# Kernel optimization log

Measured on AMD Instinct MI355X. Metric: run time of the kernel, lower is better.

Reference implementation:

```python
import jax, jax.numpy as jnp
import numpy as np

D_MODEL, H, D_K, D_V, D_FF = 1024, 16, 64, 64, 4096
B, L = 2, 2048
EPS = 1e-5


def layer_norm(x, g, b):
    mu = jnp.mean(x, axis=-1, keepdims=True)
    var = jnp.mean(jnp.square(x - mu), axis=-1, keepdims=True)
    return (x - mu) * jax.lax.rsqrt(var + EPS) * g + b


def setup_inputs() -> dict:
    key = jax.random.key(0)
    ks = jax.random.split(key, 12)
    s = 0.02
    x = jax.random.normal(ks[0], (B, L, D_MODEL), dtype=jnp.float32)
    Wq = jax.random.normal(ks[1], (H, D_MODEL, D_K), dtype=jnp.float32) * s
    Wk = jax.random.normal(ks[2], (H, D_MODEL, D_K), dtype=jnp.float32) * s
    Wv = jax.random.normal(ks[3], (H, D_MODEL, D_V), dtype=jnp.float32) * s
    bq = jnp.zeros((H, D_K), dtype=jnp.float32)
    bk = jnp.zeros((H, D_K), dtype=jnp.float32)
    bv = jnp.zeros((H, D_V), dtype=jnp.float32)
    Wo = jax.random.normal(ks[4], (H * D_V, D_MODEL), dtype=jnp.float32) * s
    W1 = jax.random.normal(ks[5], (D_MODEL, D_FF), dtype=jnp.float32) * s
    b1 = jnp.zeros((D_FF,), dtype=jnp.float32)
    W2 = jax.random.normal(ks[6], (D_FF, D_MODEL), dtype=jnp.float32) * s
    ln1_g = jnp.ones((D_MODEL,), dtype=jnp.float32)
    ln1_b = jnp.zeros((D_MODEL,), dtype=jnp.float32)
    ln2_g = jnp.ones((D_MODEL,), dtype=jnp.float32)
    ln2_b = jnp.zeros((D_MODEL,), dtype=jnp.float32)
    return dict(x=x, Wq=Wq, bq=bq, Wk=Wk, bk=bk, Wv=Wv, bv=bv, Wo=Wo,
                ln1_g=ln1_g, ln1_b=ln1_b, W1=W1, b1=b1, W2=W2,
                ln2_g=ln2_g, ln2_b=ln2_b)


def reference(x, Wq, bq, Wk, bk, Wv, bv, Wo, ln1_g, ln1_b, W1, b1, W2, ln2_g, ln2_b):
    # Batched multi-head attention (all heads at once, equivalent to the
    # per-head Python loop in the original module).
    Q = jnp.einsum('bld,hdk->bhlk', x, Wq) + bq[None, :, None, :]
    K = jnp.einsum('bld,hdk->bhlk', x, Wk) + bk[None, :, None, :]
    V = jnp.einsum('bld,hdv->bhlv', x, Wv) + bv[None, :, None, :]
    scores = jnp.einsum('bhlk,bhmk->bhlm', Q, K) * (1.0 / jnp.sqrt(jnp.float32(D_K)))
    attn = jax.nn.softmax(scores, axis=-1)
    O = jnp.einsum('bhlm,bhmv->bhlv', attn, V)        # [b,h,l,dv]
    O = jnp.transpose(O, (0, 2, 1, 3)).reshape(x.shape[0], x.shape[1], H * D_V)
    mha = O @ Wo                                       # [b,l,d_model]
    # residual + LayerNorm (dropout_prob=0 -> identity)
    h1 = layer_norm(x + mha, ln1_g, ln1_b)
    ff = jax.nn.relu(h1 @ W1 + b1) @ W2
    return layer_norm(h1 + ff, ln2_g, ln2_b)
```

## Files before the change

### kernel.cpp

```cpp
#include <hip/hip_runtime.h>

typedef unsigned short u16;
typedef unsigned int u32;
typedef short bf16x8 __attribute__((ext_vector_type(8)));
typedef float f32x4 __attribute__((ext_vector_type(4)));
typedef unsigned int u32x2 __attribute__((ext_vector_type(2)));
typedef unsigned int u32x4 __attribute__((ext_vector_type(4)));

#define D_MODEL 1024
#define NH 16
#define DK 64
#define DFF 4096
#define BATCH 2
#define SEQ 2048
#define BL (BATCH*SEQ)
#define NQKV 3072
#define Q_SCALE 0.18033688011f

__device__ __forceinline__ float bfraw2f(u16 u) {
    union { u32 i; float f; } c; c.i = ((u32)u) << 16; return c.f;
}
__device__ __forceinline__ u16 f2bfraw(float f) {
    union { float f; u32 i; } c; c.f = f;
    u32 i = c.i;
    u32 lsb = (i >> 16) & 1u;
    i += 0x7fffu + lsb;
    return (u16)(i >> 16);
}
__device__ __forceinline__ u32 fasu(float f) {
    union { float f; u32 i; } c; c.f = f; return c.i;
}
__device__ __forceinline__ u32 pack_bf2(float lo, float hi) {
    return __builtin_amdgcn_perm(fasu(hi) + 0x8000u, fasu(lo) + 0x8000u,
                                 0x07060302u);
}
__device__ __forceinline__ void gload_lds16(const u16* g, u16* l) {
    __builtin_amdgcn_global_load_lds(
        (const __attribute__((address_space(1))) void*)g,
        (__attribute__((address_space(3))) void*)l, 16, 0, 0);
}

__global__ __launch_bounds__(256) void cast_f32_bf16(const float* __restrict__ in,
                                                     u16* __restrict__ out) {
    int i = (blockIdx.x * 256 + threadIdx.x) * 4;
    f32x4 v = *(const f32x4*)&in[i];
#pragma unroll
    for (int j = 0; j < 4; j++) out[i + j] = f2bfraw(v[j]);
}


__global__ __launch_bounds__(256) void transpose2d(const float* __restrict__ in,
                                                   u16* __restrict__ out,
                                                   int R, int C) {
    __shared__ u16 t[64][65];
    int c0 = blockIdx.x * 64, r0 = blockIdx.y * 64;
    int col = threadIdx.x & 63, rr = threadIdx.x >> 6;
    for (int i = rr; i < 64; i += 4)
        t[i][col] = f2bfraw(in[(size_t)(r0 + i) * C + c0 + col]);
    __syncthreads();
    for (int i = rr; i < 64; i += 4)
        out[(size_t)(c0 + i) * R + r0 + col] = t[col][i];
}

__global__ __launch_bounds__(256) void transpose_wqkv(const float* __restrict__ Wq,
                                                      const float* __restrict__ Wk,
                                                      const float* __restrict__ Wv,
                                                      u16* __restrict__ out) {
    __shared__ u16 t[64][65];
    int d0 = blockIdx.x * 64;
    int h = blockIdx.y;
    int ms = blockIdx.z;
    const float* W = (ms == 0) ? Wq : (ms == 1) ? Wk : Wv;
    const float* src = W + (size_t)h * D_MODEL * DK;
    int col = threadIdx.x & 63, rr = threadIdx.x >> 6;
    for (int i = rr; i < 64; i += 4)
        t[i][col] = f2bfraw(src[(size_t)(d0 + i) * DK + col]);
    __syncthreads();
    u16* dst = out + (size_t)(ms * 1024 + h * 64) * D_MODEL;
    for (int i = rr; i < 64; i += 4)
        dst[(size_t)i * D_MODEL + d0 + col] = t[col][i];
}

__global__ __launch_bounds__(256) void concat_bias(const float* __restrict__ bq,
                                                   const float* __restrict__ bk,
                                                   const float* __restrict__ bv,
                                                   float* __restrict__ out) {
    int i = blockIdx.x * 256 + threadIdx.x;
    out[i] = (i < 1024) ? bq[i] : (i < 2048) ? bk[i - 1024] : bv[i - 2048];
}


template <int BM, int BN, int T, int OUT_F32, int RELU, int HASBIAS, int SPLITK,
          int SCALEQ, int VSTORE>
__global__ __launch_bounds__(T, 2) void gemm3(const u16* __restrict__ A,
                                              const u16* __restrict__ Bt,
                                              const float* __restrict__ bias,
                                              void* __restrict__ Cout,
                                              u16* __restrict__ vtout,
                                              int M, int N, int K) {
    constexpr int WGN = BN / 64;
    constexpr int WGM = (T / 64) / WGN;
    constexpr int PWM = BM / WGM;
    constexpr int MF = PWM / 16;
    __shared__ __attribute__((aligned(16))) u16 As[2][BM * 64];
    __shared__ __attribute__((aligned(16))) u16 Bs[2][BN * 64];
    const int tid = threadIdx.x;
    const int lane = tid & 63, wid = tid >> 6;
    const int quad = lane >> 4, l16 = lane & 15;

    int nwg = gridDim.x * gridDim.y;
    int flat = blockIdx.y * gridDim.x + blockIdx.x;
    if ((nwg & 7) == 0) {
        int q = nwg >> 3;
        flat = (flat & 7) * q + (flat >> 3);
    }
    const int m0 = (flat % gridDim.x) * BM;
    const int n0 = (flat / gridDim.x) * BN;

    const int z = (SPLITK > 1) ? blockIdx.z : 0;
    const int Klen = K / SPLITK;
    const int NT = Klen / 64;
    const int kb0 = z * Klen;

    const int wrow = (wid / WGN) * PWM;
    const int wcol = (wid % WGN) * 64;

    f32x4 acc[MF][4];
#pragma unroll
    for (int i = 0; i < MF; i++)
#pragma unroll
        for (int j = 0; j < 4; j++) acc[i][j] = (f32x4){0.f, 0.f, 0.f, 0.f};

    auto stage = [&](int kb, int slot) {
#pragma unroll
        for (int p = 0; p < (BM * 8) / T; p++) {
            int ew = p * T + wid * 64;
            int e = ew + lane;
            int row = e >> 3, ch = e & 7;
            gload_lds16(&A[(size_t)(m0 + row) * K + kb + ((ch ^ (row & 7)) * 8)],
                        &As[slot][ew * 8]);
        }
#pragma unroll
        for (int p = 0; p < (BN * 8) / T; p++) {
            int ew = p * T + wid * 64;
            int e = ew + lane;
            int row = e >> 3, ch = e & 7;
            gload_lds16(&Bt[(size_t)(n0 + row) * K + kb + ((ch ^ (row & 7)) * 8)],
                        &Bs[slot][ew * 8]);
        }
    };

    stage(kb0, 0);
    if (NT > 1) stage(kb0 + 64, 1);

    for (int t = 0; t < NT; t++) {
        if (t + 1 < NT) {
            asm volatile("s_waitcnt vmcnt(8)" ::: "memory");
        } else {
            asm volatile("s_waitcnt vmcnt(0)" ::: "memory");
        }
        __builtin_amdgcn_s_barrier();
        __builtin_amdgcn_sched_barrier(0);

        const u16* as = As[t & 1];
        const u16* bs = Bs[t & 1];
        __builtin_amdgcn_s_setprio(1);
        bf16x8 bfr[4][2];
#pragma unroll
        for (int j = 0; j < 4; j++) {
            int rb = wcol + j * 16 + l16;
#pragma unroll
            for (int kh = 0; kh < 2; kh++)
                bfr[j][kh] = *(const bf16x8*)&bs[rb * 64 + (((kh * 4 + quad) ^ (rb & 7)) * 8)];
        }
#pragma unroll
        for (int i = 0; i < MF; i++) {
            int ra = wrow + i * 16 + l16;
            bf16x8 a0 = *(const bf16x8*)&as[ra * 64 + ((quad ^ (ra & 7)) * 8)];
            bf16x8 a1 = *(const bf16x8*)&as[ra * 64 + (((4 + quad) ^ (ra & 7)) * 8)];
#pragma unroll
            for (int j = 0; j < 4; j++) {
                acc[i][j] = __builtin_amdgcn_mfma_f32_16x16x32_bf16(a0, bfr[j][0], acc[i][j], 0, 0, 0);
                acc[i][j] = __builtin_amdgcn_mfma_f32_16x16x32_bf16(a1, bfr[j][1], acc[i][j], 0, 0, 0);
            }
        }
        __builtin_amdgcn_s_setprio(0);
        __builtin_amdgcn_sched_barrier(0);
        __builtin_amdgcn_s_barrier();
        __builtin_amdgcn_sched_barrier(0);
        if (t + 2 < NT) stage(kb0 + (t + 2) * 64, t & 1);
    }

    if (VSTORE && n0 >= 2048) {
#pragma unroll
        for (int i = 0; i < MF; i++) {
            int row0 = m0 + wrow + i * 16 + quad * 4;
            int bb = row0 >> 11, l = row0 & 2047;
#pragma unroll
            for (int j = 0; j < 4; j++) {
                int col = n0 + wcol + j * 16 + l16;
                float bv = HASBIAS ? bias[col] : 0.f;
                int dv = col - 2048;
                u32x2 w;
                w.x = pack_bf2(acc[i][j][0] + bv, acc[i][j][1] + bv);
                w.y = pack_bf2(acc[i][j][2] + bv, acc[i][j][3] + bv);
                *(u32x2*)&vtout[((size_t)(bb * 1024 + dv)) * 2048 + l] = w;
            }
        }
        return;
    }

    float* outf = (float*)Cout + (size_t)z * M * N;
#pragma unroll
    for (int i = 0; i < MF; i++) {
#pragma unroll
        for (int j = 0; j < 4; j++) {
#pragma unroll
            for (int r = 0; r < 4; r++) {
                int row = m0 + wrow + i * 16 + quad * 4 + r;
                int col = n0 + wcol + j * 16 + l16;
                float v = acc[i][j][r];
                if (HASBIAS) v += bias[col];
                if (RELU) v = v > 0.f ? v : 0.f;
                if (SCALEQ && col < 1024) v *= Q_SCALE;
                if (OUT_F32)
                    outf[(size_t)row * N + col] = v;
                else
                    ((u16*)Cout)[(size_t)row * N + col] = f2bfraw(v);
            }
        }
    }
}

__global__ __launch_bounds__(512, 4) void attn_kernel(const u16* __restrict__ qkv,
                                                      const u16* __restrict__ vt,
                                                      u16* __restrict__ O) {
    __shared__ __attribute__((aligned(16))) u16 Ks[2][128 * 64];
    __shared__ __attribute__((aligned(16))) u16 Vs[64 * 128];

    const int tid = threadIdx.x;
    const int lane = tid & 63, wid = tid >> 6;
    const int quad = lane >> 4, l16 = lane & 15;
    const int sw = l16 & 7;
    const int b = blockIdx.z, h = blockIdx.y;
    const int q0 = blockIdx.x * 128 + wid * 16;

    const size_t qrow = (size_t)(b * SEQ + q0 + l16) * NQKV + h * DK;
    const bf16x8 qf0 = *(const bf16x8*)&qkv[qrow + quad * 8];
    const bf16x8 qf1 = *(const bf16x8*)&qkv[qrow + 32 + quad * 8];

    const u16* Kbase = qkv + (size_t)(b * SEQ) * NQKV + D_MODEL + h * DK;
    const u16* Vbase = vt + (size_t)((b * NH + h) * DK) * SEQ;

    f32x4 oacc[4];
#pragma unroll
    for (int d = 0; d < 4; d++) oacc[d] = (f32x4){0.f, 0.f, 0.f, 0.f};
    float lr = 0.f;
    const f32x4 Z = {0.f, 0.f, 0.f, 0.f};

    auto stage_k = [&](int kt2, int buf) {
#pragma unroll
        for (int p = 0; p < 2; p++) {
            int seg = p * 8 + wid;
            int row = seg * 8 + (lane >> 3);
            int chunk = (lane & 7) ^ (lane >> 3);
            gload_lds16(&Kbase[(size_t)(kt2 + row) * NQKV + chunk * 8],
                        &Ks[buf][seg * 512]);
        }
    };
    bf16x8 vreg[2];
    auto load_v = [&](int kt2) {
#pragma unroll
        for (int p = 0; p < 2; p++) {
            int s = p * 512 + tid;
            vreg[p] = *(const bf16x8*)&Vbase[(size_t)(s >> 4) * SEQ + kt2 + (s & 15) * 8];
        }
    };
    stage_k(0, 0);
    load_v(0);

    for (int t = 0; t < SEQ / 128; t++) {
        const int kt = t * 128;
#pragma unroll
        for (int p = 0; p < 2; p++) {
            int s = p * 512 + tid;
            int vr = s >> 4, vc = s & 15;
            int chunkA = (vc >> 2) * 4 + (vc & 1) * 2;
            int rem = ((vc >> 1) & 1) * 4;
            u32x4 kv = __builtin_bit_cast(u32x4, vreg[p]);
            *(u32x2*)&Vs[vr * 128 + ((chunkA ^ (vr & 7)) * 8) + rem] =
                (u32x2){kv.x, kv.y};
            *(u32x2*)&Vs[vr * 128 + (((chunkA + 1) ^ (vr & 7)) * 8) + rem] =
                (u32x2){kv.z, kv.w};
        }
        __syncthreads();

        if (t + 1 < SEQ / 128) {
            stage_k(kt + 128, (t + 1) & 1);
            load_v(kt + 128);
        }

        const u16* kb = Ks[t & 1];

        f32x4 sacc[8];
        __builtin_amdgcn_s_setprio(1);
#pragma unroll
        for (int nt = 0; nt < 8; nt++) {
            const u16* krow = &kb[(nt * 16 + l16) * 64];
            bf16x8 kf0 = *(const bf16x8*)&krow[(quad ^ sw) * 8];
            bf16x8 kf1 = *(const bf16x8*)&krow[((4 + quad) ^ sw) * 8];
            f32x4 s0 = __builtin_amdgcn_mfma_f32_16x16x32_bf16(kf0, qf0, Z, 0, 0, 0);
            sacc[nt] = __builtin_amdgcn_mfma_f32_16x16x32_bf16(kf1, qf1, s0, 0, 0, 0);
        }
        __builtin_amdgcn_s_setprio(0);

        u32 wreg[8][2];
#pragma unroll
        for (int nt = 0; nt < 8; nt++) {
            float p0 = __builtin_amdgcn_exp2f(sacc[nt][0]);
            float p1 = __builtin_amdgcn_exp2f(sacc[nt][1]);
            float p2 = __builtin_amdgcn_exp2f(sacc[nt][2]);
            float p3 = __builtin_amdgcn_exp2f(sacc[nt][3]);
            lr += (p0 + p1) + (p2 + p3);
            wreg[nt][0] = pack_bf2(p0, p1);
            wreg[nt][1] = pack_bf2(p2, p3);
        }

        __builtin_amdgcn_s_setprio(1);
#pragma unroll
        for (int ks = 0; ks < 4; ks++) {
            u32x4 pw = (u32x4){wreg[2 * ks][0], wreg[2 * ks][1],
                               wreg[2 * ks + 1][0], wreg[2 * ks + 1][1]};
            bf16x8 pf = __builtin_bit_cast(bf16x8, pw);
#pragma unroll
            for (int d = 0; d < 4; d++) {
                bf16x8 vf = *(const bf16x8*)&Vs[(d * 16 + l16) * 128 +
                                                (((ks * 4 + quad) ^ sw) * 8)];
                oacc[d] = __builtin_amdgcn_mfma_f32_16x16x32_bf16(vf, pf, oacc[d], 0, 0, 0);
            }
        }
        __builtin_amdgcn_s_setprio(0);
        __syncthreads();
    }

    lr += __shfl_xor(lr, 16, 64);
    lr += __shfl_xor(lr, 32, 64);
    float iv = 1.f / lr;

    size_t row = (size_t)(b * SEQ + q0 + l16);
#pragma unroll
    for (int d = 0; d < 4; d++) {
        float o0 = oacc[d][0] * iv, o1 = oacc[d][1] * iv;
        float o2 = oacc[d][2] * iv, o3 = oacc[d][3] * iv;
        u32x2 w;
        w.x = ((u32)f2bfraw(o1) << 16) | f2bfraw(o0);
        w.y = ((u32)f2bfraw(o3) << 16) | f2bfraw(o2);
        *(u32x2*)&O[row * D_MODEL + h * DK + d * 16 + quad * 4] = w;
    }
}

__global__ __launch_bounds__(256) void ln3_kernel(const float* __restrict__ xa,
                                                  const float* __restrict__ xb,
                                                  const float* __restrict__ xc,
                                                  const float* __restrict__ g,
                                                  const float* __restrict__ be,
                                                  u16* __restrict__ out_bf,
                                                  float* __restrict__ out_f) {
    int row = blockIdx.x;
    int tid = threadIdx.x;
    const float* pa = xa + (size_t)row * D_MODEL;
    const float* pb = xb + (size_t)row * D_MODEL;
    const float* pc = xc + (size_t)row * D_MODEL;
    int c = tid * 4;
    f32x4 av = *(const f32x4*)&pa[c];
    f32x4 bv = *(const f32x4*)&pb[c];
    f32x4 cv = *(const f32x4*)&pc[c];
    float v[4];
    float s = 0.f, ss = 0.f;
#pragma unroll
    for (int i = 0; i < 4; i++) {
        v[i] = av[i] + bv[i] + cv[i];
        s += v[i];
        ss += v[i] * v[i];
    }
#pragma unroll
    for (int off = 32; off; off >>= 1) {
        s += __shfl_down(s, off, 64);
        ss += __shfl_down(ss, off, 64);
    }
    __shared__ float red[8];
    int wid = tid >> 6, lane = tid & 63;
    if (lane == 0) { red[wid] = s; red[4 + wid] = ss; }
    __syncthreads();
    if (tid == 0) {
        red[0] = red[0] + red[1] + red[2] + red[3];
        red[4] = red[4] + red[5] + red[6] + red[7];
    }
    __syncthreads();
    float mu = red[0] * (1.f / D_MODEL);
    float var = red[4] * (1.f / D_MODEL) - mu * mu;
    float rs = rsqrtf(var + 1e-5f);
#pragma unroll
    for (int i = 0; i < 4; i++) {
        float o = (v[i] - mu) * rs * g[c + i] + be[c + i];
        if (out_f) out_f[(size_t)row * D_MODEL + c + i] = o;
        if (out_bf) out_bf[(size_t)row * D_MODEL + c + i] = f2bfraw(o);
    }
}

extern "C" void kernel_launch(void* const* d_in, const int* in_sizes, int n_in,
                              void* d_out, int out_size, void* d_ws, size_t ws_size,
                              hipStream_t stream) {
    const float* x   = (const float*)d_in[0];
    const float* Wq  = (const float*)d_in[1];
    const float* bq  = (const float*)d_in[2];
    const float* Wk  = (const float*)d_in[3];
    const float* bk  = (const float*)d_in[4];
    const float* Wv  = (const float*)d_in[5];
    const float* bv  = (const float*)d_in[6];
    const float* Wo  = (const float*)d_in[7];
    const float* g1  = (const float*)d_in[8];
    const float* be1 = (const float*)d_in[9];
    const float* W1  = (const float*)d_in[10];
    const float* b1  = (const float*)d_in[11];
    const float* W2  = (const float*)d_in[12];
    const float* g2  = (const float*)d_in[13];
    const float* be2 = (const float*)d_in[14];

    char* w = (char*)d_ws;
    auto alloc = [&](size_t bytes) {
        char* p = w;
        w += (bytes + 255) & ~(size_t)255;
        return p;
    };
    u16* wqkv_t = (u16*)alloc((size_t)NQKV * D_MODEL * 2);
    u16* wo_t   = (u16*)alloc((size_t)D_MODEL * D_MODEL * 2);
    u16* w1_t   = (u16*)alloc((size_t)DFF * D_MODEL * 2);
    u16* w2_t   = (u16*)alloc((size_t)D_MODEL * DFF * 2);
    float* bqkv = (float*)alloc((size_t)NQKV * 4);
    u16* x_bf   = (u16*)alloc((size_t)BL * D_MODEL * 2);
    u16* qkvbuf = (u16*)alloc((size_t)BL * NQKV * 2);
    u16* vtbuf  = (u16*)alloc((size_t)BATCH * NH * DK * SEQ * 2);
    u16* obuf   = (u16*)alloc((size_t)BL * D_MODEL * 2);
    float* mha_p = (float*)alloc((size_t)2 * BL * D_MODEL * 4);
    u16* h1_bf  = (u16*)alloc((size_t)BL * D_MODEL * 2);
    float* h1_f = (float*)alloc((size_t)BL * D_MODEL * 4);
    u16* ffa    = (u16*)alloc((size_t)BL * DFF * 2);
    float* ffb_p = (float*)alloc((size_t)2 * BL * D_MODEL * 4);

    cast_f32_bf16<<<dim3(BL * D_MODEL / 1024), 256, 0, stream>>>(x, x_bf);
    transpose_wqkv<<<dim3(16, 16, 3), 256, 0, stream>>>(Wq, Wk, Wv, wqkv_t);
    transpose2d<<<dim3(16, 16), 256, 0, stream>>>(Wo, wo_t, 1024, 1024);
    transpose2d<<<dim3(64, 16), 256, 0, stream>>>(W1, w1_t, 1024, 4096);
    transpose2d<<<dim3(16, 64), 256, 0, stream>>>(W2, w2_t, 4096, 1024);
    concat_bias<<<dim3(12), 256, 0, stream>>>(bq, bk, bv, bqkv);

    gemm3<256, 256, 512, 0, 0, 1, 1, 1, 1><<<dim3(16, 12), 512, 0, stream>>>(
        x_bf, wqkv_t, bqkv, qkvbuf, vtbuf, BL, NQKV, D_MODEL);
    attn_kernel<<<dim3(16, 16, 2), 512, 0, stream>>>(qkvbuf, vtbuf, obuf);
    gemm3<128, 128, 256, 1, 0, 0, 2, 0, 0><<<dim3(32, 8, 2), 256, 0, stream>>>(
        obuf, wo_t, nullptr, mha_p, nullptr, BL, D_MODEL, D_MODEL);
    ln3_kernel<<<dim3(BL), 256, 0, stream>>>(x, mha_p, mha_p + (size_t)BL * D_MODEL,
                                             g1, be1, h1_bf, h1_f);
    gemm3<256, 256, 512, 0, 1, 1, 1, 0, 0><<<dim3(16, 16), 512, 0, stream>>>(
        h1_bf, w1_t, b1, ffa, nullptr, BL, DFF, D_MODEL);
    gemm3<128, 128, 256, 1, 0, 0, 2, 0, 0><<<dim3(32, 8, 2), 256, 0, stream>>>(
        ffa, w2_t, nullptr, ffb_p, nullptr, BL, D_MODEL, DFF);
    ln3_kernel<<<dim3(BL), 256, 0, stream>>>(h1_f, ffb_p, ffb_p + (size_t)BL * D_MODEL,
                                             g2, be2, nullptr, (float*)d_out);
}
```

Measured before the change: 369.7 us.

## Restructure GEMM main loop to 4-stage 32-wide K pipeline with split staging

```diff
diff --git a/kernel.cpp b/kernel.cpp
--- a/kernel.cpp
+++ b/kernel.cpp
@@ -92,7 +92,7 @@
 
 template <int BM, int BN, int T, int OUT_F32, int RELU, int HASBIAS, int SPLITK,
           int SCALEQ, int VSTORE>
-__global__ __launch_bounds__(T, 2) void gemm3(const u16* __restrict__ A,
+__global__ __launch_bounds__(T, 2) void gemm4(const u16* __restrict__ A,
                                               const u16* __restrict__ Bt,
                                               const float* __restrict__ bias,
                                               void* __restrict__ Cout,
@@ -102,8 +102,9 @@
     constexpr int WGM = (T / 64) / WGN;
     constexpr int PWM = BM / WGM;
     constexpr int MF = PWM / 16;
-    __shared__ __attribute__((aligned(16))) u16 As[2][BM * 64];
-    __shared__ __attribute__((aligned(16))) u16 Bs[2][BN * 64];
+    constexpr int MH = MF / 2;
+    __shared__ __attribute__((aligned(16))) u16 As[4][BM * 32];
+    __shared__ __attribute__((aligned(16))) u16 Bs[4][BN * 32];
     const int tid = threadIdx.x;
     const int lane = tid & 63, wid = tid >> 6;
     const int quad = lane >> 4, l16 = lane & 15;
@@ -119,7 +120,7 @@
 
     const int z = (SPLITK > 1) ? blockIdx.z : 0;
     const int Klen = K / SPLITK;
-    const int NT = Klen / 64;
+    const int NT = Klen / 32;
     const int kb0 = z * Klen;
 
     const int wrow = (wid / WGN) * PWM;
@@ -131,64 +132,80 @@
 #pragma unroll
         for (int j = 0; j < 4; j++) acc[i][j] = (f32x4){0.f, 0.f, 0.f, 0.f};
 
-    auto stage = [&](int kb, int slot) {
-#pragma unroll
-        for (int p = 0; p < (BM * 8) / T; p++) {
-            int ew = p * T + wid * 64;
-            int e = ew + lane;
-            int row = e >> 3, ch = e & 7;
-            gload_lds16(&A[(size_t)(m0 + row) * K + kb + ((ch ^ (row & 7)) * 8)],
-                        &As[slot][ew * 8]);
-        }
-#pragma unroll
-        for (int p = 0; p < (BN * 8) / T; p++) {
-            int ew = p * T + wid * 64;
-            int e = ew + lane;
-            int row = e >> 3, ch = e & 7;
-            gload_lds16(&Bt[(size_t)(n0 + row) * K + kb + ((ch ^ (row & 7)) * 8)],
-                        &Bs[slot][ew * 8]);
+    auto stage_A = [&](int kb, int slot) {
+#pragma unroll
+        for (int p = 0; p < 2; p++) {
+            int e = p * T + tid;
+            int row = e >> 2, ch = e & 3;
+            gload_lds16(&A[(size_t)(m0 + row) * K + kb + ((ch ^ ((row >> 1) & 3)) * 8)],
+                        &As[slot][e * 8]);
         }
     };
-
-    stage(kb0, 0);
-    if (NT > 1) stage(kb0 + 64, 1);
+    auto stage_B = [&](int kb, int slot) {
+#pragma unroll
+        for (int p = 0; p < 2; p++) {
+            int e = p * T + tid;
+            int row = e >> 2, ch = e & 3;
+            gload_lds16(&Bt[(size_t)(n0 + row) * K + kb + ((ch ^ ((row >> 1) & 3)) * 8)],
+                        &Bs[slot][e * 8]);
+        }
+    };
+
+#pragma unroll
+    for (int v = 0; v < 3; v++) {
+        stage_A(kb0 + v * 32, v);
+        stage_B(kb0 + v * 32, v);
+    }
 
     for (int t = 0; t < NT; t++) {
-        if (t + 1 < NT) {
-            asm volatile("s_waitcnt vmcnt(8)" ::: "memory");
-        } else {
-            asm volatile("s_waitcnt vmcnt(0)" ::: "memory");
-        }
+        int rem = NT - 1 - t;
+        if (rem >= 2)      asm volatile("s_waitcnt vmcnt(8)" ::: "memory");
+        else if (rem == 1) asm volatile("s_waitcnt vmcnt(4)" ::: "memory");
+        else               asm volatile("s_waitcnt vmcnt(0)" ::: "memory");
         __builtin_amdgcn_s_barrier();
-        __builtin_amdgcn_sched_barrier(0);
-
-        const u16* as = As[t & 1];
-        const u16* bs = Bs[t & 1];
-        __builtin_amdgcn_s_setprio(1);
-        bf16x8 bfr[4][2];
+
+        const u16* as = As[t & 3];
+        const u16* bs = Bs[t & 3];
+        const int tp = t + 3;
+
+        if (tp < NT) stage_A(kb0 + tp * 32, tp & 3);
+        bf16x8 bfr[4];
 #pragma unroll
         for (int j = 0; j < 4; j++) {
             int rb = wcol + j * 16 + l16;
-#pragma unroll
-            for (int kh = 0; kh < 2; kh++)
-                bfr[j][kh] = *(const bf16x8*)&bs[rb * 64 + (((kh * 4 + quad) ^ (rb & 7)) * 8)];
-        }
-#pragma unroll
-        for (int i = 0; i < MF; i++) {
+            bfr[j] = *(const bf16x8*)&bs[rb * 32 + ((quad ^ ((rb >> 1) & 3)) * 8)];
+        }
+        bf16x8 afr[MH];
+#pragma unroll
+        for (int i = 0; i < MH; i++) {
             int ra = wrow + i * 16 + l16;
-            bf16x8 a0 = *(const bf16x8*)&as[ra * 64 + ((quad ^ (ra & 7)) * 8)];
-            bf16x8 a1 = *(const bf16x8*)&as[ra * 64 + (((4 + quad) ^ (ra & 7)) * 8)];
-#pragma unroll
-            for (int j = 0; j < 4; j++) {
-                acc[i][j] = __builtin_amdgcn_mfma_f32_16x16x32_bf16(a0, bfr[j][0], acc[i][j], 0, 0, 0);
-                acc[i][j] = __builtin_amdgcn_mfma_f32_16x16x32_bf16(a1, bfr[j][1], acc[i][j], 0, 0, 0);
-            }
-        }
+            afr[i] = *(const bf16x8*)&as[ra * 32 + ((quad ^ ((ra >> 1) & 3)) * 8)];
+        }
+        __builtin_amdgcn_s_setprio(1);
+#pragma unroll
+        for (int i = 0; i < MH; i++)
+#pragma unroll
+            for (int j = 0; j < 4; j++)
+                acc[i][j] = __builtin_amdgcn_mfma_f32_16x16x32_bf16(
+                    afr[i], bfr[j], acc[i][j], 0, 0, 0);
         __builtin_amdgcn_s_setprio(0);
-        __builtin_amdgcn_sched_barrier(0);
         __builtin_amdgcn_s_barrier();
-        __builtin_amdgcn_sched_barrier(0);
-        if (t + 2 < NT) stage(kb0 + (t + 2) * 64, t & 1);
+
+        if (tp < NT) stage_B(kb0 + tp * 32, tp & 3);
+        bf16x8 afr2[MH];
+#pragma unroll
+        for (int i = 0; i < MH; i++) {
+            int ra = wrow + (MH + i) * 16 + l16;
+            afr2[i] = *(const bf16x8*)&as[ra * 32 + ((quad ^ ((ra >> 1) & 3)) * 8)];
+        }
+        __builtin_amdgcn_s_setprio(1);
+#pragma unroll
+        for (int i = 0; i < MH; i++)
+#pragma unroll
+            for (int j = 0; j < 4; j++)
+                acc[MH + i][j] = __builtin_amdgcn_mfma_f32_16x16x32_bf16(
+                    afr2[i], bfr[j], acc[MH + i][j], 0, 0, 0);
+        __builtin_amdgcn_s_setprio(0);
     }
 
     if (VSTORE && n0 >= 2048) {
@@ -455,16 +472,16 @@
     transpose2d<<<dim3(16, 64), 256, 0, stream>>>(W2, w2_t, 4096, 1024);
     concat_bias<<<dim3(12), 256, 0, stream>>>(bq, bk, bv, bqkv);
 
-    gemm3<256, 256, 512, 0, 0, 1, 1, 1, 1><<<dim3(16, 12), 512, 0, stream>>>(
+    gemm4<256, 256, 512, 0, 0, 1, 1, 1, 1><<<dim3(16, 12), 512, 0, stream>>>(
         x_bf, wqkv_t, bqkv, qkvbuf, vtbuf, BL, NQKV, D_MODEL);
     attn_kernel<<<dim3(16, 16, 2), 512, 0, stream>>>(qkvbuf, vtbuf, obuf);
-    gemm3<128, 128, 256, 1, 0, 0, 2, 0, 0><<<dim3(32, 8, 2), 256, 0, stream>>>(
+    gemm4<128, 128, 256, 1, 0, 0, 2, 0, 0><<<dim3(32, 8, 2), 256, 0, stream>>>(
         obuf, wo_t, nullptr, mha_p, nullptr, BL, D_MODEL, D_MODEL);
     ln3_kernel<<<dim3(BL), 256, 0, stream>>>(x, mha_p, mha_p + (size_t)BL * D_MODEL,
                                              g1, be1, h1_bf, h1_f);
-    gemm3<256, 256, 512, 0, 1, 1, 1, 0, 0><<<dim3(16, 16), 512, 0, stream>>>(
+    gemm4<256, 256, 512, 0, 1, 1, 1, 0, 0><<<dim3(16, 16), 512, 0, stream>>>(
         h1_bf, w1_t, b1, ffa, nullptr, BL, DFF, D_MODEL);
-    gemm3<128, 128, 256, 1, 0, 0, 2, 0, 0><<<dim3(32, 8, 2), 256, 0, stream>>>(
+    gemm4<128, 128, 256, 1, 0, 0, 2, 0, 0><<<dim3(32, 8, 2), 256, 0, stream>>>(
         ffa, w2_t, nullptr, ffb_p, nullptr, BL, D_MODEL, DFF);
     ln3_kernel<<<dim3(BL), 256, 0, stream>>>(h1_f, ffb_p, ffb_p + (size_t)BL * D_MODEL,
                                              g2, be2, nullptr, (float*)d_out);
```

Result: slower. 419.9 us (+13.6%).
